# Optimization experiments

Hardware: AMD Instinct MI355X
Metric: run time of the kernel (lower is better)

Reference implementation:

```python
import jax, jax.numpy as jnp
import numpy as np

INF = 100000000.0
TOPK = 13
ALPHA = 1
BETA = 6


def box_cxcywh_to_xyxy(b):
    cx, cy, w, h = jnp.split(b, 4, axis=-1)
    return jnp.concatenate([cx - 0.5 * w, cy - 0.5 * h, cx + 0.5 * w, cy + 0.5 * h], axis=-1)


def generalized_box_iou(boxes1, boxes2):
    # boxes1: [N,4] xyxy, boxes2: [G,4] xyxy -> [N,G]
    area1 = (boxes1[:, 2] - boxes1[:, 0]) * (boxes1[:, 3] - boxes1[:, 1])
    area2 = (boxes2[:, 2] - boxes2[:, 0]) * (boxes2[:, 3] - boxes2[:, 1])
    lt = jnp.maximum(boxes1[:, None, :2], boxes2[None, :, :2])
    rb = jnp.minimum(boxes1[:, None, 2:], boxes2[None, :, 2:])
    wh = jnp.clip(rb - lt, 0.0)
    inter = wh[..., 0] * wh[..., 1]
    union = area1[:, None] + area2[None, :] - inter
    iou = inter / union
    lt_e = jnp.minimum(boxes1[:, None, :2], boxes2[None, :, :2])
    rb_e = jnp.maximum(boxes1[:, None, 2:], boxes2[None, :, 2:])
    wh_e = jnp.clip(rb_e - lt_e, 0.0)
    area_e = wh_e[..., 0] * wh_e[..., 1]
    return iou - (area_e - union) / area_e


def _assign_one(cls_logits, bbox_pred, gt_boxes, gt_labels):
    # cls_logits [N,C], bbox_pred [N,4] cxcywh, gt_boxes [G,4] cxcywh, gt_labels [G]
    N = bbox_pred.shape[0]
    G = gt_boxes.shape[0]
    scores = jax.nn.sigmoid(cls_logits)
    overlaps = -generalized_box_iou(box_cxcywh_to_xyxy(bbox_pred), box_cxcywh_to_xyxy(gt_boxes))  # [N,G]
    bbox_scores = scores[:, gt_labels]                       # [N,G] gather per-gt class score
    alignment = bbox_scores ** ALPHA * overlaps ** BETA      # [N,G]
    # per-gt topk over queries
    cand_metrics, cand_idxs = jax.lax.top_k(alignment.T, TOPK)  # [G,K]
    is_pos = cand_metrics > 0
    vals = jnp.take_along_axis(overlaps.T, cand_idxs, axis=1)   # [G,K]
    rows = jnp.broadcast_to(jnp.arange(G)[:, None], (G, TOPK))
    cols = jnp.where(is_pos, cand_idxs, N)  # out-of-bounds col -> dropped
    oinf = jnp.full((G, N), -INF, dtype=overlaps.dtype)
    oinf = oinf.at[rows, cols].set(vals, mode='drop')
    max_overlaps = oinf.max(axis=0)     # [N]
    argmax_overlaps = oinf.argmax(axis=0)
    pos = max_overlaps != -INF
    assigned_gt_inds = jnp.where(pos, argmax_overlaps + 1, 0)
    assign_metrics = jnp.where(pos, alignment[jnp.arange(N), argmax_overlaps], 0.0)
    assigned_labels = jnp.where(pos, gt_labels[argmax_overlaps], -1)
    return assigned_gt_inds, assigned_labels, assign_metrics


def setup_inputs() -> dict:
    key = jax.random.key(0)
    k1, k2, k3, k4 = jax.random.split(key, 4)
    bs, N, C, G = 16, 4000, 80, 300
    return {
        'pred_logits': jax.random.normal(k1, (bs, N, C), dtype=jnp.float32),
        'pred_boxes': jax.random.uniform(k2, (bs, N, 4), dtype=jnp.float32, minval=0.05, maxval=0.95),
        'gt_boxes': jax.random.uniform(k3, (bs, G, 4), dtype=jnp.float32, minval=0.05, maxval=0.95),
        'gt_labels': jax.random.randint(k4, (bs, G), 0, C),
    }


def reference(pred_logits, pred_boxes, gt_boxes, gt_labels):
    # Fixed-shape equivalent of matched_list: assigned_gt_inds[b,q] == 0 means
    # background; k>0 means query q matched to gt k-1 (same semantics as the
    # (valid_query_idx, valid_assigned_gt_inds) pairs in the torch code).
    return jax.vmap(_assign_one)(pred_logits, pred_boxes, gt_boxes, gt_labels)
```

## Files before the change

kernel.cpp:

```cpp
#include <hip/hip_runtime.h>

#define NPRED  4000
#define NGROUP 1000
#define NGT    300
#define NCLS   80
#define TOPKK  13
#define NCHUNK 63

typedef unsigned long long u64;

__device__ __forceinline__ float frcp(float x) { return __builtin_amdgcn_rcpf(x); }
__device__ __forceinline__ float fexp(float x) {
    return __builtin_amdgcn_exp2f(x * 1.44269504088896341f);
}

__device__ __forceinline__ float neg_giou_x(float4 p, float gx1, float gy1,
                                            float gx2, float gy2, float garea) {
    float pa  = (p.z - p.x) * (p.w - p.y);
    float whx = fmaxf(fminf(p.z, gx2) - fmaxf(p.x, gx1), 0.0f);
    float why = fmaxf(fminf(p.w, gy2) - fmaxf(p.y, gy1), 0.0f);
    float inter = whx * why;
    float uni = pa + garea - inter;
    float iou = inter * frcp(uni);
    float wex = fmaxf(p.z, gx2) - fminf(p.x, gx1);
    float wey = fmaxf(p.w, gy2) - fminf(p.y, gy1);
    float area_e = wex * wey;
    return (area_e - uni) * frcp(area_e) - iou;
}

__device__ __forceinline__ float4 to_xyxy(float4 pb) {
    return make_float4(pb.x - 0.5f * pb.z, pb.y - 0.5f * pb.w,
                       pb.x + 0.5f * pb.z, pb.y + 0.5f * pb.w);
}

__device__ __forceinline__ float sigmoid_fast(float x) {
    return frcp(1.0f + fexp(-x));
}

__device__ __forceinline__ float pow6(float x) {
    float x2 = x * x;
    float x4 = x2 * x2;
    return x2 * x4;
}

__device__ __forceinline__ unsigned ord_float(float f) {
    unsigned u = __float_as_uint(f);
    return u ^ ((unsigned)(((int)u) >> 31) | 0x80000000u);
}

__global__ void init_keys(u64* keys, int n) {
    int i = blockIdx.x * blockDim.x + threadIdx.x;
    if (i < n) keys[i] = 0ULL;
}

__global__ __launch_bounds__(256) void sig_transpose(const float* __restrict__ logits,
                                                     const float4* __restrict__ pboxes,
                                                     float* __restrict__ st,
                                                     float4* __restrict__ pxyxy,
                                                     u64* __restrict__ keys,
                                                     int total_keys) {
    const int tid = threadIdx.x;
    const int gid = blockIdx.x * 256 + tid;
    if (gid < total_keys) keys[gid] = 0ULL;

    const int b = blockIdx.x / NCHUNK;
    const int n0 = (blockIdx.x % NCHUNK) * 64;
    const int nval = (NPRED - n0 < 64) ? (NPRED - n0) : 64;

    if (tid < 64 && tid < nval) {
        pxyxy[(size_t)b * NPRED + n0 + tid] =
            to_xyxy(pboxes[(size_t)b * NPRED + n0 + tid]);
    }

    __shared__ float tile[NCLS][64 + 1];

    const float4* src = (const float4*)(logits + ((size_t)b * NPRED + n0) * NCLS);
    #pragma unroll
    for (int it = 0; it < 5; ++it) {
        int i4 = tid + it * 256;
        int p = i4 / 20;
        int c = i4 * 4 - p * 80;
        if (p < nval) {
            float4 v = src[i4];
            tile[c + 0][p] = sigmoid_fast(v.x);
            tile[c + 1][p] = sigmoid_fast(v.y);
            tile[c + 2][p] = sigmoid_fast(v.z);
            tile[c + 3][p] = sigmoid_fast(v.w);
        }
    }
    __syncthreads();
    float* dstbase = st + (size_t)b * NCLS * NPRED + n0;
    #pragma unroll
    for (int it = 0; it < 5; ++it) {
        int w4 = tid + it * 256;
        int c = w4 >> 4, r4 = (w4 & 15) * 4;
        if (r4 < nval) {
            float4 v = make_float4(tile[c][r4], tile[c][r4 + 1],
                                   tile[c][r4 + 2], tile[c][r4 + 3]);
            *(float4*)(dstbase + (size_t)c * NPRED + r4) = v;
        }
    }
}

template <bool PRE>
__global__ __launch_bounds__(256) void topk_scatter(const float* __restrict__ logits,
                                                    const float* __restrict__ st,
                                                    const float4* __restrict__ pboxes,
                                                    const float4* __restrict__ pxyxy,
                                                    const float4* __restrict__ gboxes,
                                                    const int* __restrict__ glabels,
                                                    u64* __restrict__ keys) {
    const int blk = blockIdx.x;
    const int b = blk / NGT;
    const int g = blk - b * NGT;
    const int tid = threadIdx.x;

    __shared__ float s_key[NPRED];
    __shared__ float s_rv[8];
    __shared__ int   s_ri[8];
    __shared__ int   s_win[TOPKK];
    __shared__ float s_winv[TOPKK];

    float4 gb = gboxes[b * NGT + g];
    const int lab = glabels[b * NGT + g];
    const float gx1 = gb.x - 0.5f * gb.z;
    const float gy1 = gb.y - 0.5f * gb.w;
    const float gx2 = gb.x + 0.5f * gb.z;
    const float gy2 = gb.y + 0.5f * gb.w;
    const float garea = (gx2 - gx1) * (gy2 - gy1);

    const float* lg = logits + (size_t)b * NPRED * NCLS + lab;
    const float* srow = st + ((size_t)b * NCLS + lab) * NPRED;
    const float4* srow4 = (const float4*)srow;
    const float4* pbb = pboxes + (size_t)b * NPRED;
    const float4* pxr = pxyxy + (size_t)b * NPRED;

    float b1v = -1.0f, b2v = -1.0f;
    int b1i = 0x7FFFFFFF, b2i = 0x7FFFFFFF;
    #pragma unroll
    for (int j = 0; j < 4; ++j) {
        int grp = tid + j * 256;
        if (grp < NGROUP) {
            int n0 = grp * 4;
            float s0, s1, s2, s3;
            float4 p0, p1, p2, p3;
            if (PRE) {
                float4 s4 = srow4[grp];
                s0 = s4.x; s1 = s4.y; s2 = s4.z; s3 = s4.w;
                p0 = pxr[n0]; p1 = pxr[n0 + 1]; p2 = pxr[n0 + 2]; p3 = pxr[n0 + 3];
            } else {
                s0 = sigmoid_fast(lg[(size_t)(n0 + 0) * NCLS]);
                s1 = sigmoid_fast(lg[(size_t)(n0 + 1) * NCLS]);
                s2 = sigmoid_fast(lg[(size_t)(n0 + 2) * NCLS]);
                s3 = sigmoid_fast(lg[(size_t)(n0 + 3) * NCLS]);
                p0 = to_xyxy(pbb[n0]);     p1 = to_xyxy(pbb[n0 + 1]);
                p2 = to_xyxy(pbb[n0 + 2]); p3 = to_xyxy(pbb[n0 + 3]);
            }
            float v0 = s0 * pow6(neg_giou_x(p0, gx1, gy1, gx2, gy2, garea));
            float v1 = s1 * pow6(neg_giou_x(p1, gx1, gy1, gx2, gy2, garea));
            float v2 = s2 * pow6(neg_giou_x(p2, gx1, gy1, gx2, gy2, garea));
            float v3 = s3 * pow6(neg_giou_x(p3, gx1, gy1, gx2, gy2, garea));
            s_key[n0 + 0] = v0; s_key[n0 + 1] = v1;
            s_key[n0 + 2] = v2; s_key[n0 + 3] = v3;
            if (v0 > b1v)      { b2v = b1v; b2i = b1i; b1v = v0; b1i = n0; }
            else if (v0 > b2v) { b2v = v0; b2i = n0; }
            if (v1 > b1v)      { b2v = b1v; b2i = b1i; b1v = v1; b1i = n0 + 1; }
            else if (v1 > b2v) { b2v = v1; b2i = n0 + 1; }
            if (v2 > b1v)      { b2v = b1v; b2i = b1i; b1v = v2; b1i = n0 + 2; }
            else if (v2 > b2v) { b2v = v2; b2i = n0 + 2; }
            if (v3 > b1v)      { b2v = b1v; b2i = b1i; b1v = v3; b1i = n0 + 3; }
            else if (v3 > b2v) { b2v = v3; b2i = n0 + 3; }
        }
    }

    int nwin = 0;
    for (int k = 0; k < TOPKK; ++k) {
        float rv = b1v; int ri = b1i;
        #pragma unroll
        for (int off = 32; off > 0; off >>= 1) {
            float v2 = __shfl_down(rv, off, 64);
            int   i2 = __shfl_down(ri, off, 64);
            bool take = (v2 > rv) || (v2 == rv && i2 < ri);
            rv = take ? v2 : rv;
            ri = take ? i2 : ri;
        }
        const int buf = (k & 1) * 4;
        if ((tid & 63) == 0) { s_rv[buf + (tid >> 6)] = rv; s_ri[buf + (tid >> 6)] = ri; }
        __syncthreads();
        float wv = s_rv[buf]; int wi = s_ri[buf];
        #pragma unroll
        for (int w = 1; w < 4; ++w) {
            float v2 = s_rv[buf + w]; int i2 = s_ri[buf + w];
            if (v2 > wv || (v2 == wv && i2 < wi)) { wv = v2; wi = i2; }
        }
        if (!(wv > 0.0f)) break;
        if (tid == 0) { s_win[k] = wi; s_winv[k] = wv; }
        nwin = k + 1;
        if (tid == ((wi >> 2) & 255)) {
            s_key[wi] = -1.0f;
            if (b2i != 0x7FFFFFFF) {
                b1v = b2v; b1i = b2i; b2v = -1.0f; b2i = 0x7FFFFFFF;
            } else {
                b1v = -1.0f; b1i = 0x7FFFFFFF;
                #pragma unroll
                for (int jj = 0; jj < 4; ++jj) {
                    int grp = tid + jj * 256;
                    if (grp >= NGROUP) continue;
                    int n0 = grp * 4;
                    #pragma unroll
                    for (int sb = 0; sb < 4; ++sb) {
                        int n = n0 + sb;
                        float v = s_key[n];
                        if (v > b1v)      { b2v = b1v; b2i = b1i; b1v = v; b1i = n; }
                        else if (v > b2v) { b2v = v; b2i = n; }
                    }
                }
            }
        }
    }
    __syncthreads();

    if (tid < nwin) {
        int wi = s_win[tid];
        float o;
        if (PRE) {
            o = neg_giou_x(pxr[wi], gx1, gy1, gx2, gy2, garea);
        } else {
            o = neg_giou_x(to_xyxy(pbb[wi]), gx1, gy1, gx2, gy2, garea);
        }
        unsigned mbits = __float_as_uint(s_winv[tid]) >> 16;
        u64 key = ((u64)ord_float(o) << 32)
                | ((u64)(511u - (unsigned)g) << 23)
                | ((u64)mbits << 7);
        atomicMax(&keys[(size_t)b * NPRED + wi], key);
    }
}

__global__ void finalize(const int* __restrict__ glabels,
                         const u64* __restrict__ keys,
                         float* __restrict__ out, int total) {
    int i = blockIdx.x * blockDim.x + threadIdx.x;
    if (i >= total) return;
    int b = i / NPRED;
    u64 key = keys[i];
    float o0 = 0.0f, o1 = -1.0f, o2 = 0.0f;
    if (key != 0ULL) {
        int g = 511 - (int)((key >> 23) & 0x1FF);
        o0 = (float)(g + 1);
        o1 = (float)glabels[b * NGT + g];
        o2 = __uint_as_float(((unsigned)(key >> 7) & 0xFFFFu) << 16);
    }
    out[i] = o0;
    out[(size_t)total + i] = o1;
    out[(size_t)2 * total + i] = o2;
}

extern "C" void kernel_launch(void* const* d_in, const int* in_sizes, int n_in,
                              void* d_out, int out_size, void* d_ws, size_t ws_size,
                              hipStream_t stream) {
    const float* logits  = (const float*)d_in[0];
    const float4* pboxes = (const float4*)d_in[1];
    const float4* gboxes = (const float4*)d_in[2];
    const int* glabels   = (const int*)d_in[3];

    const int bs = in_sizes[3] / NGT;
    const int total = bs * NPRED;
    char* ws = (char*)d_ws;
    u64* keys   = (u64*)ws;                    ws += (size_t)total * 8;
    float* st   = (float*)ws;                  ws += (size_t)bs * NCLS * NPRED * 4;
    float4* pxy = (float4*)ws;                 ws += (size_t)total * 16;
    float* out = (float*)d_out;

    const size_t need = (size_t)(ws - (char*)d_ws);
    if (ws_size >= need) {
        sig_transpose<<<bs * NCHUNK, 256, 0, stream>>>(logits, pboxes, st, pxy,
                                                       keys, total);
        topk_scatter<true><<<bs * NGT, 256, 0, stream>>>(logits, st, pboxes, pxy,
                                                         gboxes, glabels, keys);
    } else {
        init_keys<<<(total + 255) / 256, 256, 0, stream>>>(keys, total);
        topk_scatter<false><<<bs * NGT, 256, 0, stream>>>(logits, st, pboxes, pxy,
                                                          gboxes, glabels, keys);
    }
    finalize<<<(total + 255) / 256, 256, 0, stream>>>(glabels, keys, out, total);
}
```

Measured before the change: 137.7 us.

## Extract two top-k winners per reduction round using packed 64-bit keys

Packs each alignment value and its inverted index into one 64-bit key, so a comparison is a single integer compare that also breaks ties toward the lower index. The wave reduction now keeps a running top-2 with xor shuffles, and each block-level round takes two winners, cutting the serial top-13 loop from 13 rounds to 7 and the number of barriers with it. Shared-memory stores and rescans use float4. The risk is heavier 64-bit shuffles per round and more complex owner bookkeeping when both winners belong to the same thread. Correctness relies on values being non-negative so the raw float bits order correctly.

```diff
diff --git a/kernel.cpp b/kernel.cpp
--- a/kernel.cpp
+++ b/kernel.cpp
@@ -48,6 +48,10 @@
     return u ^ ((unsigned)(((int)u) >> 31) | 0x80000000u);
 }
 
+__device__ __forceinline__ u64 pack_key(float v, int n) {
+    return ((u64)__float_as_uint(v) << 32) | (u64)(~(unsigned)n);
+}
+
 __global__ void init_keys(u64* keys, int n) {
     int i = blockIdx.x * blockDim.x + threadIdx.x;
     if (i < n) keys[i] = 0ULL;
@@ -114,12 +118,12 @@
     const int b = blk / NGT;
     const int g = blk - b * NGT;
     const int tid = threadIdx.x;
-
-    __shared__ float s_key[NPRED];
-    __shared__ float s_rv[8];
-    __shared__ int   s_ri[8];
-    __shared__ int   s_win[TOPKK];
-    __shared__ float s_winv[TOPKK];
+    const int wave = tid >> 6;
+    const int lane = tid & 63;
+
+    __shared__ __align__(16) float s_key[NPRED];
+    __shared__ u64 s_pair[2][8];
+    __shared__ u64 s_win[TOPKK];
 
     float4 gb = gboxes[b * NGT + g];
     const int lab = glabels[b * NGT + g];
@@ -135,8 +139,7 @@
     const float4* pbb = pboxes + (size_t)b * NPRED;
     const float4* pxr = pxyxy + (size_t)b * NPRED;
 
-    float b1v = -1.0f, b2v = -1.0f;
-    int b1i = 0x7FFFFFFF, b2i = 0x7FFFFFFF;
+    u64 b1 = 0ULL, b2 = 0ULL;
     #pragma unroll
     for (int j = 0; j < 4; ++j) {
         int grp = tid + j * 256;
@@ -160,60 +163,81 @@
             float v1 = s1 * pow6(neg_giou_x(p1, gx1, gy1, gx2, gy2, garea));
             float v2 = s2 * pow6(neg_giou_x(p2, gx1, gy1, gx2, gy2, garea));
             float v3 = s3 * pow6(neg_giou_x(p3, gx1, gy1, gx2, gy2, garea));
-            s_key[n0 + 0] = v0; s_key[n0 + 1] = v1;
-            s_key[n0 + 2] = v2; s_key[n0 + 3] = v3;
-            if (v0 > b1v)      { b2v = b1v; b2i = b1i; b1v = v0; b1i = n0; }
-            else if (v0 > b2v) { b2v = v0; b2i = n0; }
-            if (v1 > b1v)      { b2v = b1v; b2i = b1i; b1v = v1; b1i = n0 + 1; }
-            else if (v1 > b2v) { b2v = v1; b2i = n0 + 1; }
-            if (v2 > b1v)      { b2v = b1v; b2i = b1i; b1v = v2; b1i = n0 + 2; }
-            else if (v2 > b2v) { b2v = v2; b2i = n0 + 2; }
-            if (v3 > b1v)      { b2v = b1v; b2i = b1i; b1v = v3; b1i = n0 + 3; }
-            else if (v3 > b2v) { b2v = v3; b2i = n0 + 3; }
+            *(float4*)&s_key[n0] = make_float4(v0, v1, v2, v3);
+            u64 k0 = pack_key(v0, n0);
+            u64 k1 = pack_key(v1, n0 + 1);
+            u64 k2 = pack_key(v2, n0 + 2);
+            u64 k3 = pack_key(v3, n0 + 3);
+            if (k0 > b1)      { b2 = b1; b1 = k0; } else if (k0 > b2) b2 = k0;
+            if (k1 > b1)      { b2 = b1; b1 = k1; } else if (k1 > b2) b2 = k1;
+            if (k2 > b1)      { b2 = b1; b1 = k2; } else if (k2 > b2) b2 = k2;
+            if (k3 > b1)      { b2 = b1; b1 = k3; } else if (k3 > b2) b2 = k3;
         }
     }
 
     int nwin = 0;
-    for (int k = 0; k < TOPKK; ++k) {
-        float rv = b1v; int ri = b1i;
+    for (int k = 0; k < 7; ++k) {
+        u64 m1 = b1, m2 = b2;
         #pragma unroll
-        for (int off = 32; off > 0; off >>= 1) {
-            float v2 = __shfl_down(rv, off, 64);
-            int   i2 = __shfl_down(ri, off, 64);
-            bool take = (v2 > rv) || (v2 == rv && i2 < ri);
-            rv = take ? v2 : rv;
-            ri = take ? i2 : ri;
-        }
-        const int buf = (k & 1) * 4;
-        if ((tid & 63) == 0) { s_rv[buf + (tid >> 6)] = rv; s_ri[buf + (tid >> 6)] = ri; }
+        for (int m = 1; m < 64; m <<= 1) {
+            u64 o1 = __shfl_xor(m1, m, 64);
+            u64 o2 = __shfl_xor(m2, m, 64);
+            u64 hi = (m1 > o1) ? m1 : o1;
+            u64 lo = (m1 > o1) ? o1 : m1;
+            u64 c2 = (m2 > o2) ? m2 : o2;
+            m2 = (lo > c2) ? lo : c2;
+            m1 = hi;
+        }
+        const int buf = k & 1;
+        if (lane == 0) { s_pair[buf][wave * 2] = m1; s_pair[buf][wave * 2 + 1] = m2; }
         __syncthreads();
-        float wv = s_rv[buf]; int wi = s_ri[buf];
+        u64 t1 = 0ULL, t2 = 0ULL;
         #pragma unroll
-        for (int w = 1; w < 4; ++w) {
-            float v2 = s_rv[buf + w]; int i2 = s_ri[buf + w];
-            if (v2 > wv || (v2 == wv && i2 < wi)) { wv = v2; wi = i2; }
-        }
-        if (!(wv > 0.0f)) break;
-        if (tid == 0) { s_win[k] = wi; s_winv[k] = wv; }
-        nwin = k + 1;
-        if (tid == ((wi >> 2) & 255)) {
-            s_key[wi] = -1.0f;
-            if (b2i != 0x7FFFFFFF) {
-                b1v = b2v; b1i = b2i; b2v = -1.0f; b2i = 0x7FFFFFFF;
+        for (int w = 0; w < 8; ++w) {
+            u64 c = s_pair[buf][w];
+            if (c > t1)      { t2 = t1; t1 = c; }
+            else if (c > t2) { t2 = c; }
+        }
+        bool p1 = (unsigned)(t1 >> 32) != 0u;
+        if (!p1) break;
+        bool p2 = ((unsigned)(t2 >> 32) != 0u) && (2 * k + 1 < TOPKK);
+        if (tid == 0) {
+            s_win[2 * k] = t1;
+            if (p2) s_win[2 * k + 1] = t2;
+        }
+        nwin = 2 * k + 1 + (p2 ? 1 : 0);
+        if (!p2 || 2 * k + 1 == TOPKK - 1) {
+            if (!p2) break;
+        }
+        int n1 = (int)(~(unsigned)t1);
+        int n2 = p2 ? (int)(~(unsigned)t2) : -1;
+        bool own1 = (((n1 >> 2) & 255) == tid);
+        bool own2 = p2 && (((n2 >> 2) & 255) == tid);
+        if (own1 | own2) {
+            if (own1) s_key[n1] = 0.0f;
+            if (own2) s_key[n2] = 0.0f;
+            if (own1 && own2) {
+                b1 = 0ULL; b2 = 0ULL;
+            } else if (b2 != 0ULL) {
+                b1 = b2; b2 = 0ULL;
             } else {
-                b1v = -1.0f; b1i = 0x7FFFFFFF;
+                b1 = 0ULL;
+            }
+            if (b1 == 0ULL) {
                 #pragma unroll
                 for (int jj = 0; jj < 4; ++jj) {
                     int grp = tid + jj * 256;
                     if (grp >= NGROUP) continue;
                     int n0 = grp * 4;
-                    #pragma unroll
-                    for (int sb = 0; sb < 4; ++sb) {
-                        int n = n0 + sb;
-                        float v = s_key[n];
-                        if (v > b1v)      { b2v = b1v; b2i = b1i; b1v = v; b1i = n; }
-                        else if (v > b2v) { b2v = v; b2i = n; }
-                    }
+                    float4 q = *(const float4*)&s_key[n0];
+                    u64 c0 = pack_key(q.x, n0);
+                    u64 c1 = pack_key(q.y, n0 + 1);
+                    u64 c2k = pack_key(q.z, n0 + 2);
+                    u64 c3 = pack_key(q.w, n0 + 3);
+                    if (c0 > b1)      { b2 = b1; b1 = c0; } else if (c0 > b2) b2 = c0;
+                    if (c1 > b1)      { b2 = b1; b1 = c1; } else if (c1 > b2) b2 = c1;
+                    if (c2k > b1)     { b2 = b1; b1 = c2k; } else if (c2k > b2) b2 = c2k;
+                    if (c3 > b1)      { b2 = b1; b1 = c3; } else if (c3 > b2) b2 = c3;
                 }
             }
         }
@@ -221,14 +245,15 @@
     __syncthreads();
 
     if (tid < nwin) {
-        int wi = s_win[tid];
+        u64 t = s_win[tid];
+        int wi = (int)(~(unsigned)t);
         float o;
         if (PRE) {
             o = neg_giou_x(pxr[wi], gx1, gy1, gx2, gy2, garea);
         } else {
             o = neg_giou_x(to_xyxy(pbb[wi]), gx1, gy1, gx2, gy2, garea);
         }
-        unsigned mbits = __float_as_uint(s_winv[tid]) >> 16;
+        unsigned mbits = (unsigned)(t >> 32) >> 16;
         u64 key = ((u64)ord_float(o) << 32)
                 | ((u64)(511u - (unsigned)g) << 23)
                 | ((u64)mbits << 7);
```

After: 140.8 us. 1.02x slower.
